# Kernel tuning notes

Hardware: AMD Instinct MI355X
Metric: run time of the kernel (lower is better)

The kernel has to match this reference:

```python
import jax, jax.numpy as jnp
import numpy as np


def setup_inputs() -> dict:
    key = jax.random.key(0)
    k1, k2, k3, k4 = jax.random.split(key, 4)
    HIDDEN = 1024
    L1_CAP = 4096
    L2_CAP = 16384
    B = 4096
    return {
        "query": jax.random.normal(k1, (B, HIDDEN), dtype=jnp.float32),
        "W": jax.random.normal(k2, (HIDDEN, HIDDEN), dtype=jnp.float32) * (1.0 / np.sqrt(HIDDEN)),
        "l1": jax.random.normal(k3, (L1_CAP, HIDDEN), dtype=jnp.float32),
        "l2": jax.random.normal(k4, (L2_CAP, HIDDEN), dtype=jnp.float32),
        "l1_mask": jnp.ones((L1_CAP,), dtype=bool),
        "l2_mask": jnp.ones((L2_CAP,), dtype=bool),
        "top_k": 16,
    }


def reference(query, W, l1, l2, l1_mask, l2_mask, top_k):
    # score_proj: Linear(hidden, hidden, bias=False) -> q @ W.T
    q_proj = query @ W.T                      # [B, H]
    mem = jnp.concatenate([l1, l2], axis=0)   # [M, H]
    mask = jnp.concatenate([l1_mask, l2_mask], axis=0)  # [M]
    # masked scoring
    scores = q_proj @ mem.T                   # [B, M]
    scores = jnp.where(mask[None, :], scores, -jnp.inf)
    # top-k selection + softmax weighting (masks are all True -> k == top_k)
    vals, idx = jax.lax.top_k(scores, top_k)  # [B, K]
    soft = jax.nn.softmax(vals, axis=-1)      # [B, K]
    # gathered memory is detached in the original (mem[idx].detach())
    gathered = jax.lax.stop_gradient(mem)[idx]  # [B, K, H]
    gathered = gathered * soft[..., None]
    return gathered
```

## Files before the change

kernel.cpp:

```cpp
#include <hip/hip_runtime.h>


#define HIDDEN 1024
#define BQ     4096
#define TOPK   16
#define MTOT   20480
#define NSEG   160

typedef __attribute__((ext_vector_type(8)))  short s8v;
typedef __attribute__((ext_vector_type(4)))  float f4v;
typedef __attribute__((ext_vector_type(4)))  int   i4v;
typedef __attribute__((ext_vector_type(8)))  int   i8v;

#define WAITVM(N) asm volatile("s_waitcnt vmcnt(" #N ")" ::: "memory")

static __device__ __forceinline__ unsigned short f32_to_bf16_rne(float f) {
  unsigned u = __float_as_uint(f);
  unsigned r = 0x7FFFu + ((u >> 16) & 1u);
  return (unsigned short)((u + r) >> 16);
}
static __device__ __forceinline__ float bf16_to_f32(unsigned short h) {
  return __uint_as_float(((unsigned)h) << 16);
}
static __device__ __forceinline__ unsigned bf16_key(unsigned v) {
  return v ^ ((v >> 15) ? 0xFFFFu : 0x8000u);
}

__global__ __launch_bounds__(256) void hm_cvt_split2(
    const float* __restrict__ q, const float* __restrict__ W,
    unsigned short* __restrict__ qh, unsigned short* __restrict__ ql,
    unsigned short* __restrict__ wh, unsigned short* __restrict__ wl) {
  const int NQ = BQ * HIDDEN / 4;
  int i = blockIdx.x * 256 + threadIdx.x;
  const float* in;
  unsigned short *ho, *lo;
  int j;
  if (i < NQ) { in = q; j = i;      ho = qh; lo = ql; }
  else        { in = W; j = i - NQ; ho = wh; lo = wl; }
  float4 x = ((const float4*)in)[j];
  ushort4 h, l;
  h.x = f32_to_bf16_rne(x.x); l.x = f32_to_bf16_rne(x.x - bf16_to_f32(h.x));
  h.y = f32_to_bf16_rne(x.y); l.y = f32_to_bf16_rne(x.y - bf16_to_f32(h.y));
  h.z = f32_to_bf16_rne(x.z); l.z = f32_to_bf16_rne(x.z - bf16_to_f32(h.z));
  h.w = f32_to_bf16_rne(x.w); l.w = f32_to_bf16_rne(x.w - bf16_to_f32(h.w));
  ((ushort4*)ho)[j] = h;
  ((ushort4*)lo)[j] = l;
}

__global__ __launch_bounds__(256) void hm_cvt_fp8_all(
    const float* __restrict__ qpf, const float* __restrict__ l1,
    const float* __restrict__ l2, unsigned char* __restrict__ qp8,
    unsigned char* __restrict__ mem8) {
  const int NQ8 = BQ * HIDDEN / 8;
  int i = blockIdx.x * 256 + threadIdx.x;
  const float* src;
  unsigned char* dst;
  int j;
  if (i < NQ8) { src = qpf + (size_t)i * 8; dst = qp8; j = i; }
  else {
    j = i - NQ8;
    int row = j >> 7, colg = j & 127;
    src = (row < 4096) ? (l1 + (size_t)row * HIDDEN + colg * 8)
                       : (l2 + (size_t)(row - 4096) * HIDDEN + colg * 8);
    dst = mem8;
  }
  float4 x = ((const float4*)src)[0], y = ((const float4*)src)[1];
  int u0 = __builtin_amdgcn_cvt_pk_fp8_f32(x.x, x.y, 0, false);
  u0     = __builtin_amdgcn_cvt_pk_fp8_f32(x.z, x.w, u0, true);
  int u1 = __builtin_amdgcn_cvt_pk_fp8_f32(y.x, y.y, 0, false);
  u1     = __builtin_amdgcn_cvt_pk_fp8_f32(y.z, y.w, u1, true);
  uint2 o; o.x = (unsigned)u0; o.y = (unsigned)u1;
  ((uint2*)dst)[j] = o;
}

__global__ __launch_bounds__(256) void hm_gemm_split3(
    const unsigned short* __restrict__ Ahi, const unsigned short* __restrict__ Alo,
    const unsigned short* __restrict__ Bhi, const unsigned short* __restrict__ Blo,
    float* __restrict__ Cf, int N, int K) {
  __shared__ unsigned short lds[2][16384];
  const int tid = threadIdx.x, lane = tid & 63, w = tid >> 6;
  const int m0 = blockIdx.x * 128, n0 = blockIdx.y * 128;
  const int wr = (w >> 1) * 64, wc = (w & 1) * 64;
  f4v acc[4][4] = {};
  const unsigned short* plane = (w == 0) ? Ahi : (w == 1) ? Alo : (w == 2) ? Bhi : Blo;
  const int gbase = (w < 2) ? m0 : n0;
  const int kg = lane >> 4, r16 = lane & 15;
  const int NT = K / 32;

  auto STAGE = [&](int cur, int t) {
#pragma unroll
    for (int is = 0; is < 8; ++is) {
      int slot = is * 64 + lane;
      int row = slot >> 2, kgs = slot & 3;
      const unsigned short* gp = plane + (size_t)(gbase + row) * K + (t * 32 + kgs * 8);
      unsigned short* lp = &lds[cur][(w * 512 + is * 64) * 8];
      __builtin_amdgcn_global_load_lds(
          (const __attribute__((address_space(1))) unsigned int*)gp,
          (__attribute__((address_space(3))) unsigned int*)lp, 16, 0, 0);
    }
  };

  STAGE(0, 0);
  __syncthreads();
  for (int t = 0; t < NT; ++t) {
    int cur = t & 1;
    if (t + 1 < NT) STAGE(cur ^ 1, t + 1);

    s8v ah[4], al[4], bh[4], bl[4];
#pragma unroll
    for (int mi = 0; mi < 4; ++mi) {
      int ro = wr + mi * 16 + r16;
      ah[mi] = *(const s8v*)&lds[cur][(0 * 512 + ro * 4 + kg) * 8];
      al[mi] = *(const s8v*)&lds[cur][(1 * 512 + ro * 4 + kg) * 8];
    }
#pragma unroll
    for (int ni = 0; ni < 4; ++ni) {
      int ro = wc + ni * 16 + r16;
      bh[ni] = *(const s8v*)&lds[cur][(2 * 512 + ro * 4 + kg) * 8];
      bl[ni] = *(const s8v*)&lds[cur][(3 * 512 + ro * 4 + kg) * 8];
    }
#pragma unroll
    for (int mi = 0; mi < 4; ++mi)
#pragma unroll
      for (int ni = 0; ni < 4; ++ni) {
        acc[mi][ni] = __builtin_amdgcn_mfma_f32_16x16x32_bf16(ah[mi], bh[ni], acc[mi][ni], 0, 0, 0);
        acc[mi][ni] = __builtin_amdgcn_mfma_f32_16x16x32_bf16(ah[mi], bl[ni], acc[mi][ni], 0, 0, 0);
        acc[mi][ni] = __builtin_amdgcn_mfma_f32_16x16x32_bf16(al[mi], bh[ni], acc[mi][ni], 0, 0, 0);
      }
    __syncthreads();
  }
  const int cr = (lane >> 4) * 4, cc = lane & 15;
#pragma unroll
  for (int mi = 0; mi < 4; ++mi)
#pragma unroll
    for (int ni = 0; ni < 4; ++ni)
#pragma unroll
      for (int j = 0; j < 4; ++j) {
        int R = m0 + wr + mi * 16 + cr + j;
        int Cc = n0 + wc + ni * 16 + cc;
        Cf[(size_t)R * N + Cc] = acc[mi][ni][j];
      }
}

__global__ __launch_bounds__(256, 2) void hm_gemm_fp8(
    const unsigned char* __restrict__ A8, const unsigned char* __restrict__ B8,
    unsigned short* __restrict__ Cbf, unsigned short* __restrict__ segMax,
    int N, int K) {
  __shared__ __align__(16) char smem[65536];
  const int tid = threadIdx.x, lane = tid & 63, w = tid >> 6;
  const int m0 = blockIdx.x * 128, n0 = blockIdx.y * 128;
  const int wr = (w >> 1) * 64, wc = (w & 1) * 64;
  const int r16 = lane & 15, kg = lane >> 4;
  const int sc = 0x7F7F7F7F;
  const int NT = 8;

  f4v acc[4][4] = {};

  const int lrow = lane >> 3;
  const int lkc  = (lane & 7) ^ lrow;

  auto STAGE = [&](int buf, int t) {
    char* bA = smem + buf * 32768;
    char* bB = bA + 16384;
    int k0 = t * 128;
#pragma unroll
    for (int ii = 0; ii < 4; ++ii) {
      int r0 = w * 32 + ii * 8;
      const unsigned char* gA = A8 + (size_t)(m0 + r0 + lrow) * K + k0 + lkc * 16;
      __builtin_amdgcn_global_load_lds(
          (const __attribute__((address_space(1))) unsigned int*)gA,
          (__attribute__((address_space(3))) unsigned int*)(bA + r0 * 128),
          16, 0, 0);
      const unsigned char* gB = B8 + (size_t)(n0 + r0 + lrow) * K + k0 + lkc * 16;
      __builtin_amdgcn_global_load_lds(
          (const __attribute__((address_space(1))) unsigned int*)gB,
          (__attribute__((address_space(3))) unsigned int*)(bB + r0 * 128),
          16, 0, 0);
    }
  };

  STAGE(0, 0);
#pragma unroll
  for (int t = 0; t < NT; ++t) {
    if (t + 1 < NT) { STAGE((t + 1) & 1, t + 1); WAITVM(8); }
    else            { WAITVM(0); }
    __builtin_amdgcn_s_barrier();

    const char* bA = smem + (t & 1) * 32768;
    const char* bB = bA + 16384;
    i8v a[4], b[4];
#pragma unroll
    for (int mi = 0; mi < 4; ++mi) {
      int row = wr + mi * 16 + r16;
      int x = row & 7;
      i4v lo = *(const i4v*)(bA + (row * 8 + ((kg * 2)     ^ x)) * 16);
      i4v hi = *(const i4v*)(bA + (row * 8 + ((kg * 2 + 1) ^ x)) * 16);
      a[mi][0]=lo[0]; a[mi][1]=lo[1]; a[mi][2]=lo[2]; a[mi][3]=lo[3];
      a[mi][4]=hi[0]; a[mi][5]=hi[1]; a[mi][6]=hi[2]; a[mi][7]=hi[3];
    }
#pragma unroll
    for (int ni = 0; ni < 4; ++ni) {
      int row = wc + ni * 16 + r16;
      int x = row & 7;
      i4v lo = *(const i4v*)(bB + (row * 8 + ((kg * 2)     ^ x)) * 16);
      i4v hi = *(const i4v*)(bB + (row * 8 + ((kg * 2 + 1) ^ x)) * 16);
      b[ni][0]=lo[0]; b[ni][1]=lo[1]; b[ni][2]=lo[2]; b[ni][3]=lo[3];
      b[ni][4]=hi[0]; b[ni][5]=hi[1]; b[ni][6]=hi[2]; b[ni][7]=hi[3];
    }
    __builtin_amdgcn_s_setprio(1);
#pragma unroll
    for (int mi = 0; mi < 4; ++mi)
#pragma unroll
      for (int ni = 0; ni < 4; ++ni)
        acc[mi][ni] = __builtin_amdgcn_mfma_scale_f32_16x16x128_f8f6f4(
            a[mi], b[ni], acc[mi][ni], 0, 0, 0, sc, 0, sc);
    __builtin_amdgcn_s_setprio(0);

    asm volatile("s_waitcnt lgkmcnt(0)" ::: "memory");
    __builtin_amdgcn_sched_barrier(0);
    __builtin_amdgcn_s_barrier();
  }

  short* ldsC = (short*)smem;
  const int cr = kg * 4, cc = r16;
#pragma unroll
  for (int mi = 0; mi < 4; ++mi)
#pragma unroll
    for (int ni = 0; ni < 4; ++ni)
#pragma unroll
      for (int j = 0; j < 4; ++j) {
        int row = wr + mi * 16 + cr + j;
        int col = wc + ni * 16 + cc;
        ldsC[row * 128 + col] = (short)f32_to_bf16_rne(acc[mi][ni][j]);
      }
  __syncthreads();
#pragma unroll
  for (int it = 0; it < 8; ++it) {
    int idx = it * 256 + tid;
    int row = idx >> 4, c16 = idx & 15;
    uint4 v = *(const uint4*)(ldsC + row * 128 + c16 * 8);
    *(uint4*)(Cbf + (size_t)(m0 + row) * N + n0 + c16 * 8) = v;
    float m8 = bf16_to_f32((unsigned short)(v.x & 0xffff));
    m8 = fmaxf(m8, bf16_to_f32((unsigned short)(v.x >> 16)));
    m8 = fmaxf(m8, bf16_to_f32((unsigned short)(v.y & 0xffff)));
    m8 = fmaxf(m8, bf16_to_f32((unsigned short)(v.y >> 16)));
    m8 = fmaxf(m8, bf16_to_f32((unsigned short)(v.z & 0xffff)));
    m8 = fmaxf(m8, bf16_to_f32((unsigned short)(v.z >> 16)));
    m8 = fmaxf(m8, bf16_to_f32((unsigned short)(v.w & 0xffff)));
    m8 = fmaxf(m8, bf16_to_f32((unsigned short)(v.w >> 16)));
#pragma unroll
    for (int mask = 1; mask < 16; mask <<= 1) m8 = fmaxf(m8, __shfl_xor(m8, mask));
    if ((tid & 15) == 0)
      segMax[(size_t)(m0 + row) * NSEG + (n0 >> 7)] = f32_to_bf16_rne(m8);
  }
}

__global__ __launch_bounds__(256) void hm_topk(
    const unsigned short* __restrict__ scores,
    const unsigned short* __restrict__ segMax, int* __restrict__ stIdx) {
  int tid = threadIdx.x, lane = tid & 63, w = tid >> 6;
  int b = blockIdx.x * 4 + w;
  const unsigned short* sm = segMax + (size_t)b * NSEG;
  const unsigned* rowp = (const unsigned*)(scores + (size_t)b * MTOT);

  unsigned q[8];
#pragma unroll
  for (int i = 0; i < 8; ++i) q[i] = 0;

  auto push = [&](unsigned p) {
    if (p > q[7]) {
      q[7] = p;
#pragma unroll
      for (int i = 7; i > 0; --i) {
        unsigned hi = q[i - 1] > q[i] ? q[i - 1] : q[i];
        unsigned lo = q[i - 1] > q[i] ? q[i] : q[i - 1];
        q[i - 1] = hi; q[i] = lo;
      }
    }
  };

  unsigned sk[3];
#pragma unroll
  for (int g = 0; g < 3; ++g) {
    int s = g * 64 + lane;
    sk[g] = (s < NSEG) ? bf16_key(sm[s]) : 0;
    if (s < NSEG) push((sk[g] << 16) | s);
  }
  unsigned tau = 0;
#pragma unroll
  for (int r = 0; r < TOPK; ++r) {
    unsigned m = q[0];
#pragma unroll
    for (int mk = 1; mk < 64; mk <<= 1) {
      unsigned o = (unsigned)__shfl_xor((int)m, mk);
      m = m > o ? m : o;
    }
    if (q[0] == m) {
#pragma unroll
      for (int i = 0; i < 7; ++i) q[i] = q[i + 1];
      q[7] = 0;
    }
    tau = m;
  }
  tau >>= 16;

#pragma unroll
  for (int i = 0; i < 8; ++i) q[i] = 0;
#pragma unroll
  for (int g = 0; g < 3; ++g) {
    int s0 = g * 64 + lane;
    unsigned long long mk = __ballot(s0 < NSEG && sk[g] >= tau);
    while (mk) {
      int src = __ffsll(mk) - 1;
      mk &= mk - 1;
      int s = g * 64 + src;
      unsigned d = rowp[s * 64 + lane];
      unsigned v0 = d & 0xffffu, v1 = d >> 16;
      int col = s * 128 + lane * 2;
      push((bf16_key(v0) << 16) | col);
      push((bf16_key(v1) << 16) | (col + 1));
    }
  }

  unsigned keep = 0;
#pragma unroll
  for (int r = 0; r < TOPK; ++r) {
    unsigned m = q[0];
#pragma unroll
    for (int mk = 1; mk < 64; mk <<= 1) {
      unsigned o = (unsigned)__shfl_xor((int)m, mk);
      m = m > o ? m : o;
    }
    if (q[0] == m) {
#pragma unroll
      for (int i = 0; i < 7; ++i) q[i] = q[i + 1];
      q[7] = 0;
    }
    if (lane == r) keep = m;
  }
  if (lane < TOPK) stIdx[b * TOPK + lane] = (int)(keep & 0xffffu);
}

__global__ __launch_bounds__(256) void hm_refine_gather(
    const float* __restrict__ qp, const int* __restrict__ stIdx,
    const float* __restrict__ l1, const float* __restrict__ l2,
    float* __restrict__ out) {
  __shared__ float vals[TOPK], wts[TOPK], red[TOPK][4], ssum[1];
  __shared__ int rankOf[TOPK], sidx[TOPK];
  int b = blockIdx.x, tid = threadIdx.x;
  int lane = tid & 63, w = tid >> 6;
  if (tid < TOPK) sidx[tid] = stIdx[b * TOPK + tid];
  float4 q4 = ((const float4*)(qp + (size_t)b * HIDDEN))[tid];
  __syncthreads();

  float4 m4[TOPK];
  float p[TOPK];
#pragma unroll
  for (int k = 0; k < TOPK; ++k) {
    int idx = sidx[k];
    const float4* mr = (idx < 4096) ? (const float4*)(l1 + (size_t)idx * HIDDEN)
                                    : (const float4*)(l2 + (size_t)(idx - 4096) * HIDDEN);
    m4[k] = mr[tid];
    p[k] = q4.x * m4[k].x + q4.y * m4[k].y + q4.z * m4[k].z + q4.w * m4[k].w;
  }
#pragma unroll
  for (int k = 0; k < TOPK; ++k)
#pragma unroll
    for (int mask = 1; mask < 64; mask <<= 1) p[k] += __shfl_xor(p[k], mask);
  if (lane == 0)
#pragma unroll
    for (int k = 0; k < TOPK; ++k) red[k][w] = p[k];
  __syncthreads();
  if (tid < TOPK) vals[tid] = red[tid][0] + red[tid][1] + red[tid][2] + red[tid][3];
  __syncthreads();
  if (tid < TOPK) {
    float vt = vals[tid];
    int it = sidx[tid], r = 0;
    float m = vals[0];
#pragma unroll
    for (int j = 0; j < TOPK; ++j) {
      float vj = vals[j];
      m = fmaxf(m, vj);
      r += (vj > vt || (vj == vt && sidx[j] < it)) ? 1 : 0;
    }
    rankOf[tid] = r;
    wts[tid] = expf(vt - m);
  }
  __syncthreads();
  if (tid == 0) {
    float s = 0.f;
#pragma unroll
    for (int j = 0; j < TOPK; ++j) s += wts[j];
    ssum[0] = s;
  }
  __syncthreads();
  float inv = 1.0f / ssum[0];
#pragma unroll
  for (int k = 0; k < TOPK; ++k) {
    float wt = wts[k] * inv;
    int r = rankOf[k];
    float4 x = m4[k];
    x.x *= wt; x.y *= wt; x.z *= wt; x.w *= wt;
    ((float4*)out)[((size_t)b * TOPK + r) * 256 + tid] = x;
  }
}

extern "C" void kernel_launch(void* const* d_in, const int* in_sizes, int n_in,
                              void* d_out, int out_size, void* d_ws, size_t ws_size,
                              hipStream_t stream) {
  const float* query = (const float*)d_in[0];
  const float* W     = (const float*)d_in[1];
  const float* l1    = (const float*)d_in[2];
  const float* l2    = (const float*)d_in[3];
  float* out = (float*)d_out;

  const size_t MiB = 1024 * 1024;
  char* ws = (char*)d_ws;
  unsigned short* qh  = (unsigned short*)(ws + 0);
  unsigned short* ql  = (unsigned short*)(ws + 8 * MiB);
  unsigned short* wh  = (unsigned short*)(ws + 16 * MiB);
  unsigned short* wl  = (unsigned short*)(ws + 18 * MiB);
  float*          qpf = (float*)(ws + 20 * MiB);
  unsigned char*  qp8 = (unsigned char*)(ws + 0);
  int*            stIdx = (int*)(ws + 36 * MiB);

  unsigned short* scores  = (unsigned short*)d_out;
  unsigned short* segMax  = (unsigned short*)((char*)d_out + 192 * MiB);
  unsigned char*  mem8    = (unsigned char*)d_out + 200 * MiB;

  hm_cvt_split2<<<dim3((BQ * HIDDEN + HIDDEN * HIDDEN) / 1024), dim3(256), 0, stream>>>(
      query, W, qh, ql, wh, wl);
  hm_gemm_split3<<<dim3(BQ / 128, HIDDEN / 128), dim3(256), 0, stream>>>(
      qh, ql, wh, wl, qpf, HIDDEN, HIDDEN);
  hm_cvt_fp8_all<<<dim3((BQ * HIDDEN + MTOT * HIDDEN) / 2048), dim3(256), 0, stream>>>(
      qpf, l1, l2, qp8, mem8);

  hm_gemm_fp8<<<dim3(BQ / 128, MTOT / 128), dim3(256), 0, stream>>>(
      qp8, mem8, scores, segMax, MTOT, HIDDEN);
  hm_topk<<<dim3(BQ / 4), dim3(256), 0, stream>>>(scores, segMax, stIdx);
  hm_refine_gather<<<dim3(BQ), dim3(256), 0, stream>>>(qpf, stIdx, l1, l2, out);
}
```

Before: 278.0 us.

## Widen FP8 scoring tile to 128x160, fuse query FP8 cast into projection GEMM

The FP8 scoring GEMM now uses 128x160 tiles with a unified A/B LDS staging buffer, so there are 128 segments per row instead of 160. Each wave computes 4x5 MFMA blocks and takes the segment max straight from the accumulators, removing the scan over bf16 values read back from LDS. The projection GEMM also writes FP8 query values in its epilogue, so query no longer goes through the separate conversion pass and that extra traffic is saved. Costs are higher register and LDS use (72KB per block, which may reduce occupancy) and byte-wide scattered FP8 stores in the projection epilogue.

```diff
diff --git a/kernel.cpp b/kernel.cpp
--- a/kernel.cpp
+++ b/kernel.cpp
@@ -5,7 +5,7 @@
 #define BQ     4096
 #define TOPK   16
 #define MTOT   20480
-#define NSEG   160
+#define NSEG   128
 
 typedef __attribute__((ext_vector_type(8)))  short s8v;
 typedef __attribute__((ext_vector_type(4)))  float f4v;
@@ -47,36 +47,26 @@
   ((ushort4*)lo)[j] = l;
 }
 
-__global__ __launch_bounds__(256) void hm_cvt_fp8_all(
-    const float* __restrict__ qpf, const float* __restrict__ l1,
-    const float* __restrict__ l2, unsigned char* __restrict__ qp8,
-    unsigned char* __restrict__ mem8) {
-  const int NQ8 = BQ * HIDDEN / 8;
+__global__ __launch_bounds__(256) void hm_cvt_mem_fp8(
+    const float* __restrict__ l1, const float* __restrict__ l2,
+    unsigned char* __restrict__ out8) {
   int i = blockIdx.x * 256 + threadIdx.x;
-  const float* src;
-  unsigned char* dst;
-  int j;
-  if (i < NQ8) { src = qpf + (size_t)i * 8; dst = qp8; j = i; }
-  else {
-    j = i - NQ8;
-    int row = j >> 7, colg = j & 127;
-    src = (row < 4096) ? (l1 + (size_t)row * HIDDEN + colg * 8)
-                       : (l2 + (size_t)(row - 4096) * HIDDEN + colg * 8);
-    dst = mem8;
-  }
+  int row = i >> 7, colg = i & 127;
+  const float* src = (row < 4096) ? (l1 + (size_t)row * HIDDEN + colg * 8)
+                                  : (l2 + (size_t)(row - 4096) * HIDDEN + colg * 8);
   float4 x = ((const float4*)src)[0], y = ((const float4*)src)[1];
   int u0 = __builtin_amdgcn_cvt_pk_fp8_f32(x.x, x.y, 0, false);
   u0     = __builtin_amdgcn_cvt_pk_fp8_f32(x.z, x.w, u0, true);
   int u1 = __builtin_amdgcn_cvt_pk_fp8_f32(y.x, y.y, 0, false);
   u1     = __builtin_amdgcn_cvt_pk_fp8_f32(y.z, y.w, u1, true);
   uint2 o; o.x = (unsigned)u0; o.y = (unsigned)u1;
-  ((uint2*)dst)[j] = o;
+  ((uint2*)out8)[i] = o;
 }
 
 __global__ __launch_bounds__(256) void hm_gemm_split3(
     const unsigned short* __restrict__ Ahi, const unsigned short* __restrict__ Alo,
     const unsigned short* __restrict__ Bhi, const unsigned short* __restrict__ Blo,
-    float* __restrict__ Cf, int N, int K) {
+    float* __restrict__ Cf, unsigned char* __restrict__ C8, int N, int K) {
   __shared__ unsigned short lds[2][16384];
   const int tid = threadIdx.x, lane = tid & 63, w = tid >> 6;
   const int m0 = blockIdx.x * 128, n0 = blockIdx.y * 128;
@@ -138,7 +128,10 @@
       for (int j = 0; j < 4; ++j) {
         int R = m0 + wr + mi * 16 + cr + j;
         int Cc = n0 + wc + ni * 16 + cc;
-        Cf[(size_t)R * N + Cc] = acc[mi][ni][j];
+        float v = acc[mi][ni][j];
+        Cf[(size_t)R * N + Cc] = v;
+        C8[(size_t)R * N + Cc] =
+            (unsigned char)(__builtin_amdgcn_cvt_pk_fp8_f32(v, v, 0, false) & 0xff);
       }
 }
 
@@ -146,64 +139,60 @@
     const unsigned char* __restrict__ A8, const unsigned char* __restrict__ B8,
     unsigned short* __restrict__ Cbf, unsigned short* __restrict__ segMax,
     int N, int K) {
-  __shared__ __align__(16) char smem[65536];
+  __shared__ __align__(16) char smem[73728];
   const int tid = threadIdx.x, lane = tid & 63, w = tid >> 6;
-  const int m0 = blockIdx.x * 128, n0 = blockIdx.y * 128;
-  const int wr = (w >> 1) * 64, wc = (w & 1) * 64;
+  const int m0 = blockIdx.x * 128, n0 = blockIdx.y * 160;
+  const int wr = (w >> 1) * 64;
+  const int wc = (w & 1) * 80;
   const int r16 = lane & 15, kg = lane >> 4;
   const int sc = 0x7F7F7F7F;
   const int NT = 8;
 
-  f4v acc[4][4] = {};
+  f4v acc[4][5] = {};
 
   const int lrow = lane >> 3;
   const int lkc  = (lane & 7) ^ lrow;
 
   auto STAGE = [&](int buf, int t) {
-    char* bA = smem + buf * 32768;
-    char* bB = bA + 16384;
+    char* base = smem + buf * 36864;
     int k0 = t * 128;
 #pragma unroll
-    for (int ii = 0; ii < 4; ++ii) {
-      int r0 = w * 32 + ii * 8;
-      const unsigned char* gA = A8 + (size_t)(m0 + r0 + lrow) * K + k0 + lkc * 16;
+    for (int ii = 0; ii < 9; ++ii) {
+      int r0 = w * 72 + ii * 8;
+      const unsigned char* g;
+      if (r0 < 128) g = A8 + (size_t)(m0 + r0 + lrow) * K + k0 + lkc * 16;
+      else          g = B8 + (size_t)(n0 + r0 - 128 + lrow) * K + k0 + lkc * 16;
       __builtin_amdgcn_global_load_lds(
-          (const __attribute__((address_space(1))) unsigned int*)gA,
-          (__attribute__((address_space(3))) unsigned int*)(bA + r0 * 128),
+          (const __attribute__((address_space(1))) unsigned int*)g,
+          (__attribute__((address_space(3))) unsigned int*)(base + r0 * 128),
           16, 0, 0);
-      const unsigned char* gB = B8 + (size_t)(n0 + r0 + lrow) * K + k0 + lkc * 16;
-      __builtin_amdgcn_global_load_lds(
-          (const __attribute__((address_space(1))) unsigned int*)gB,
-          (__attribute__((address_space(3))) unsigned int*)(bB + r0 * 128),
-          16, 0, 0);
     }
   };
 
   STAGE(0, 0);
 #pragma unroll
   for (int t = 0; t < NT; ++t) {
-    if (t + 1 < NT) { STAGE((t + 1) & 1, t + 1); WAITVM(8); }
+    if (t + 1 < NT) { STAGE((t + 1) & 1, t + 1); WAITVM(9); }
     else            { WAITVM(0); }
     __builtin_amdgcn_s_barrier();
 
-    const char* bA = smem + (t & 1) * 32768;
-    const char* bB = bA + 16384;
-    i8v a[4], b[4];
+    const char* base = smem + (t & 1) * 36864;
+    i8v a[4], b[5];
 #pragma unroll
     for (int mi = 0; mi < 4; ++mi) {
       int row = wr + mi * 16 + r16;
       int x = row & 7;
-      i4v lo = *(const i4v*)(bA + (row * 8 + ((kg * 2)     ^ x)) * 16);
-      i4v hi = *(const i4v*)(bA + (row * 8 + ((kg * 2 + 1) ^ x)) * 16);
+      i4v lo = *(const i4v*)(base + (row * 8 + ((kg * 2)     ^ x)) * 16);
+      i4v hi = *(const i4v*)(base + (row * 8 + ((kg * 2 + 1) ^ x)) * 16);
       a[mi][0]=lo[0]; a[mi][1]=lo[1]; a[mi][2]=lo[2]; a[mi][3]=lo[3];
       a[mi][4]=hi[0]; a[mi][5]=hi[1]; a[mi][6]=hi[2]; a[mi][7]=hi[3];
     }
 #pragma unroll
-    for (int ni = 0; ni < 4; ++ni) {
-      int row = wc + ni * 16 + r16;
+    for (int ni = 0; ni < 5; ++ni) {
+      int row = 128 + wc + ni * 16 + r16;
       int x = row & 7;
-      i4v lo = *(const i4v*)(bB + (row * 8 + ((kg * 2)     ^ x)) * 16);
-      i4v hi = *(const i4v*)(bB + (row * 8 + ((kg * 2 + 1) ^ x)) * 16);
+      i4v lo = *(const i4v*)(base + (row * 8 + ((kg * 2)     ^ x)) * 16);
+      i4v hi = *(const i4v*)(base + (row * 8 + ((kg * 2 + 1) ^ x)) * 16);
       b[ni][0]=lo[0]; b[ni][1]=lo[1]; b[ni][2]=lo[2]; b[ni][3]=lo[3];
       b[ni][4]=hi[0]; b[ni][5]=hi[1]; b[ni][6]=hi[2]; b[ni][7]=hi[3];
     }
@@ -211,7 +200,7 @@
 #pragma unroll
     for (int mi = 0; mi < 4; ++mi)
 #pragma unroll
-      for (int ni = 0; ni < 4; ++ni)
+      for (int ni = 0; ni < 5; ++ni)
         acc[mi][ni] = __builtin_amdgcn_mfma_scale_f32_16x16x128_f8f6f4(
             a[mi], b[ni], acc[mi][ni], 0, 0, 0, sc, 0, sc);
     __builtin_amdgcn_s_setprio(0);
@@ -222,36 +211,35 @@
   }
 
   short* ldsC = (short*)smem;
+  float* partMax = (float*)(smem + 40960);
   const int cr = kg * 4, cc = r16;
 #pragma unroll
   for (int mi = 0; mi < 4; ++mi)
 #pragma unroll
-    for (int ni = 0; ni < 4; ++ni)
-#pragma unroll
-      for (int j = 0; j < 4; ++j) {
-        int row = wr + mi * 16 + cr + j;
+    for (int j = 0; j < 4; ++j) {
+      int row = wr + mi * 16 + cr + j;
+      float m = acc[mi][0][j];
+#pragma unroll
+      for (int ni = 1; ni < 5; ++ni) m = fmaxf(m, acc[mi][ni][j]);
+#pragma unroll
+      for (int mask = 1; mask < 16; mask <<= 1) m = fmaxf(m, __shfl_xor(m, mask));
+      if (r16 == 0) partMax[row * 2 + (w & 1)] = m;
+#pragma unroll
+      for (int ni = 0; ni < 5; ++ni) {
         int col = wc + ni * 16 + cc;
-        ldsC[row * 128 + col] = (short)f32_to_bf16_rne(acc[mi][ni][j]);
+        ldsC[row * 160 + col] = (short)f32_to_bf16_rne(acc[mi][ni][j]);
       }
-  __syncthreads();
-#pragma unroll
-  for (int it = 0; it < 8; ++it) {
+    }
+  __syncthreads();
+  if (tid < 128)
+    segMax[(size_t)(m0 + tid) * NSEG + blockIdx.y] =
+        f32_to_bf16_rne(fmaxf(partMax[tid * 2], partMax[tid * 2 + 1]));
+#pragma unroll
+  for (int it = 0; it < 10; ++it) {
     int idx = it * 256 + tid;
-    int row = idx >> 4, c16 = idx & 15;
-    uint4 v = *(const uint4*)(ldsC + row * 128 + c16 * 8);
-    *(uint4*)(Cbf + (size_t)(m0 + row) * N + n0 + c16 * 8) = v;
-    float m8 = bf16_to_f32((unsigned short)(v.x & 0xffff));
-    m8 = fmaxf(m8, bf16_to_f32((unsigned short)(v.x >> 16)));
-    m8 = fmaxf(m8, bf16_to_f32((unsigned short)(v.y & 0xffff)));
-    m8 = fmaxf(m8, bf16_to_f32((unsigned short)(v.y >> 16)));
-    m8 = fmaxf(m8, bf16_to_f32((unsigned short)(v.z & 0xffff)));
-    m8 = fmaxf(m8, bf16_to_f32((unsigned short)(v.z >> 16)));
-    m8 = fmaxf(m8, bf16_to_f32((unsigned short)(v.w & 0xffff)));
-    m8 = fmaxf(m8, bf16_to_f32((unsigned short)(v.w >> 16)));
-#pragma unroll
-    for (int mask = 1; mask < 16; mask <<= 1) m8 = fmaxf(m8, __shfl_xor(m8, mask));
-    if ((tid & 15) == 0)
-      segMax[(size_t)(m0 + row) * NSEG + (n0 >> 7)] = f32_to_bf16_rne(m8);
+    int row = idx / 20, c = idx % 20;
+    uint4 v = *(const uint4*)(ldsC + row * 160 + c * 8);
+    *(uint4*)(Cbf + (size_t)(m0 + row) * N + n0 + c * 8) = v;
   }
 }
 
@@ -279,12 +267,12 @@
     }
   };
 
-  unsigned sk[3];
-#pragma unroll
-  for (int g = 0; g < 3; ++g) {
+  unsigned sk[2];
+#pragma unroll
+  for (int g = 0; g < 2; ++g) {
     int s = g * 64 + lane;
-    sk[g] = (s < NSEG) ? bf16_key(sm[s]) : 0;
-    if (s < NSEG) push((sk[g] << 16) | s);
+    sk[g] = bf16_key(sm[s]);
+    push((sk[g] << 16) | s);
   }
   unsigned tau = 0;
 #pragma unroll
@@ -307,18 +295,22 @@
 #pragma unroll
   for (int i = 0; i < 8; ++i) q[i] = 0;
 #pragma unroll
-  for (int g = 0; g < 3; ++g) {
-    int s0 = g * 64 + lane;
-    unsigned long long mk = __ballot(s0 < NSEG && sk[g] >= tau);
+  for (int g = 0; g < 2; ++g) {
+    unsigned long long mk = __ballot(sk[g] >= tau);
     while (mk) {
       int src = __ffsll(mk) - 1;
       mk &= mk - 1;
       int s = g * 64 + src;
-      unsigned d = rowp[s * 64 + lane];
-      unsigned v0 = d & 0xffffu, v1 = d >> 16;
-      int col = s * 128 + lane * 2;
-      push((bf16_key(v0) << 16) | col);
-      push((bf16_key(v1) << 16) | (col + 1));
+      unsigned d = rowp[s * 80 + lane];
+      int col = s * 160 + lane * 2;
+      push((bf16_key(d & 0xffffu) << 16) | col);
+      push((bf16_key(d >> 16) << 16) | (col + 1));
+      if (lane < 16) {
+        unsigned d2 = rowp[s * 80 + 64 + lane];
+        int c2 = s * 160 + 128 + lane * 2;
+        push((bf16_key(d2 & 0xffffu) << 16) | c2);
+        push((bf16_key(d2 >> 16) << 16) | (c2 + 1));
+      }
     }
   }
 
@@ -421,8 +413,8 @@
   unsigned short* wh  = (unsigned short*)(ws + 16 * MiB);
   unsigned short* wl  = (unsigned short*)(ws + 18 * MiB);
   float*          qpf = (float*)(ws + 20 * MiB);
-  unsigned char*  qp8 = (unsigned char*)(ws + 0);
-  int*            stIdx = (int*)(ws + 36 * MiB);
+  unsigned char*  qp8 = (unsigned char*)(ws + 40 * MiB);
+  int*            stIdx = (int*)(ws + 44 * MiB);
 
   unsigned short* scores  = (unsigned short*)d_out;
   unsigned short* segMax  = (unsigned short*)((char*)d_out + 192 * MiB);
@@ -431,11 +423,10 @@
   hm_cvt_split2<<<dim3((BQ * HIDDEN + HIDDEN * HIDDEN) / 1024), dim3(256), 0, stream>>>(
       query, W, qh, ql, wh, wl);
   hm_gemm_split3<<<dim3(BQ / 128, HIDDEN / 128), dim3(256), 0, stream>>>(
-      qh, ql, wh, wl, qpf, HIDDEN, HIDDEN);
-  hm_cvt_fp8_all<<<dim3((BQ * HIDDEN + MTOT * HIDDEN) / 2048), dim3(256), 0, stream>>>(
-      qpf, l1, l2, qp8, mem8);
-
-  hm_gemm_fp8<<<dim3(BQ / 128, MTOT / 128), dim3(256), 0, stream>>>(
+      qh, ql, wh, wl, qpf, qp8, HIDDEN, HIDDEN);
+  hm_cvt_mem_fp8<<<dim3(MTOT * HIDDEN / 2048), dim3(256), 0, stream>>>(l1, l2, mem8);
+
+  hm_gemm_fp8<<<dim3(BQ / 128, MTOT / 160), dim3(256), 0, stream>>>(
       qp8, mem8, scores, segMax, MTOT, HIDDEN);
   hm_topk<<<dim3(BQ / 4), dim3(256), 0, stream>>>(scores, segMax, stIdx);
   hm_refine_gather<<<dim3(BQ), dim3(256), 0, stream>>>(qpf, stIdx, l1, l2, out);
```

After: 873.0 us. 214% more time.
